# Kernel optimization log

Hardware: AMD Instinct MI355X
Metric: run time of the kernel (lower is better)

Reference implementation:

```python
import jax, jax.numpy as jnp
import numpy as np

H = 1024
B_SZ = 4
L = 2048


def setup_inputs() -> dict:
    key = jax.random.key(0)
    ks = jax.random.split(key, 7)
    s_in = 1.0 / np.sqrt(H)
    x = jax.random.normal(ks[0], (B_SZ, L, H), dtype=jnp.float32)
    # torch nn.Linear weights: (out_features, in_features)
    W_proj = jax.random.uniform(ks[1], (4 * H, H), minval=-s_in, maxval=s_in, dtype=jnp.float32)
    W_delta = jax.random.uniform(ks[2], (H, H), minval=-s_in, maxval=s_in, dtype=jnp.float32)
    b_delta = jax.random.uniform(ks[3], (H,), minval=-s_in, maxval=s_in, dtype=jnp.float32)
    A = 0.02 * jax.random.normal(ks[4], (1, 1, H), dtype=jnp.float32)
    Bp = 0.02 * jax.random.normal(ks[5], (1, H, 1), dtype=jnp.float32)
    D = jnp.ones((1,), dtype=jnp.float32)
    return {"x": x, "W_proj": W_proj, "A": A, "Bp": Bp, "D": D, "W_delta": W_delta, "b_delta": b_delta}


def reference(x, W_proj, A, Bp, D, W_delta, b_delta):
    # x: (b, l, h)
    h = x.shape[-1]
    proj = x @ W_proj.T                                   # (b, l, 4h)
    delta, Bs, Cs, residual = jnp.split(proj, 4, axis=-1) # each (b, l, h)
    delta = jax.nn.softplus(delta @ W_delta.T + b_delta)  # (b, l, h)
    A1 = A[0, 0]       # (h,)
    B1 = Bp[0, :, 0]   # (h,)
    # discretization: dA[b,h,l] = exp(delta*A)[b,l,h] * B1[h] (n-dim of Bp has size 1)
    dA = jnp.exp(delta * A1) * B1                         # (b, l, h), layout transposed vs torch
    # dB[b,h,0,l] = cumsum_l(delta[b,l,h] * B1[h])
    dB = jnp.cumsum(delta * B1, axis=1)                   # (b, l, h)
    # selective_scan: y[b,h,l] = sum_n (dA[b,h,l]*u[b,h,n] + dB[b,h,0,l]) * C[b,h,n]
    # sum over n distributes: y = dA * sum_n(u*C) + dB * sum_n(C)
    uC = jnp.sum(x * Cs, axis=1, keepdims=True)           # (b, 1, h)
    Csum = jnp.sum(Cs, axis=1, keepdims=True)             # (b, 1, h)
    y = dA * uC + dB * Csum                               # (b, l, h)
    return y + residual * D
```

## Files before the change

### kernel.cpp

```cpp
#include <hip/hip_runtime.h>
#include <hip/hip_bf16.h>
#include <cstdint>

#define H 1024
#define BSZ 4
#define LSEQ 2048
#define M_TOT (BSZ*LSEQ)
#define NCH 32
#define LCH (LSEQ/NCH)

typedef __attribute__((ext_vector_type(4))) float  f32x4;
typedef __attribute__((ext_vector_type(2))) float  f32x2;
typedef __attribute__((ext_vector_type(8))) __bf16 bf16x8;
typedef __attribute__((ext_vector_type(4))) __bf16 bf16x4;
typedef __attribute__((ext_vector_type(2))) __bf16 bf16x2;

typedef __attribute__((address_space(1))) unsigned int as1_u32;
typedef __attribute__((address_space(3))) unsigned int as3_u32;

__device__ __forceinline__ void gld_lds16(const void* g, const void* l) {
    as1_u32* gp = reinterpret_cast<as1_u32*>((uintptr_t)g);
    as3_u32* lp = reinterpret_cast<as3_u32*>((uint32_t)(uintptr_t)l);
    __builtin_amdgcn_global_load_lds(gp, lp, 16, 0, 0);
}

__device__ __forceinline__ float softplus_fast(float f) {
    return fmaxf(f, 0.f) + __logf(1.f + __expf(-fabsf(f)));
}

template<int KT, int MODE>
__global__ __launch_bounds__(256, 3) void gemm_bt(
    const __bf16* __restrict__ A,
    const __bf16* __restrict__ B,
    __bf16* __restrict__ O0)
{
    constexpr int K = KT * 32;
    __shared__ __align__(16) __bf16 lds[16384];

    const int tid  = threadIdx.x;
    const int lane = tid & 63;
    const int wid  = tid >> 6;
    const int wr   = (wid >> 1) * 64;
    const int wc   = (wid & 1) * 64;
    const int l15  = lane & 15;
    const int quad = lane >> 4;

    const int row0 = blockIdx.y * 128;
    const int col0 = blockIdx.x * 128;

    const int srow = lane >> 2;
    const int soct = (lane & 3) ^ ((lane >> 3) & 3);
    const __bf16* ag0 = A + (size_t)(row0 + (wid    )*16 + srow) * K + soct*8;
    const __bf16* ag1 = A + (size_t)(row0 + (wid + 4)*16 + srow) * K + soct*8;
    const __bf16* bg0 = B + (size_t)(col0 + (wid    )*16 + srow) * K + soct*8;
    const __bf16* bg1 = B + (size_t)(col0 + (wid + 4)*16 + srow) * K + soct*8;
    const int lA0 = (wid    )*512;
    const int lA1 = (wid + 4)*512;
    const int lB0 = 4096 + (wid    )*512;
    const int lB1 = 4096 + (wid + 4)*512;

    const int sw = (l15 >> 1) & 3;
    int aoff[4], boff[4];
#pragma unroll
    for (int i = 0; i < 4; ++i) {
        aoff[i] =        ((wr + i*16 + l15) * 4 + (quad ^ sw)) * 8;
        boff[i] = 4096 + ((wc + i*16 + l15) * 4 + (quad ^ sw)) * 8;
    }

    f32x4 acc[4][4] = {};

    auto stage = [&](int buf) {
        __bf16* base = lds + buf * 8192;
        gld_lds16(ag0, base + lA0);
        gld_lds16(ag1, base + lA1);
        gld_lds16(bg0, base + lB0);
        gld_lds16(bg1, base + lB1);
        ag0 += 32; ag1 += 32; bg0 += 32; bg1 += 32;
    };
    auto compute = [&](int buf) {
        const __bf16* base = lds + buf * 8192;
        bf16x8 af[4], bf[4];
#pragma unroll
        for (int i = 0; i < 4; ++i) af[i] = *(const bf16x8*)(base + aoff[i]);
#pragma unroll
        for (int j = 0; j < 4; ++j) bf[j] = *(const bf16x8*)(base + boff[j]);
#pragma unroll
        for (int i = 0; i < 4; ++i)
#pragma unroll
            for (int j = 0; j < 4; ++j)
                acc[i][j] = __builtin_amdgcn_mfma_f32_16x16x32_bf16(
                    af[i], bf[j], acc[i][j], 0, 0, 0);
    };

    stage(0);
#pragma unroll 2
    for (int kt = 0; kt < KT; ++kt) {
        __syncthreads();
        if (kt + 1 < KT) stage((kt + 1) & 1);
        compute(kt & 1);
    }

    const int colb = col0 + wc + l15;
    const int rowb = row0 + wr + quad*4;
#pragma unroll
    for (int i = 0; i < 4; ++i)
#pragma unroll
        for (int j = 0; j < 4; ++j) {
            const int col = colb + j*16;
#pragma unroll
            for (int r = 0; r < 4; ++r)
                O0[(size_t)(rowb + i*16 + r) * H + col] = (__bf16)acc[i][j][r];
        }
}


#define BAR()    asm volatile("s_barrier" ::: "memory")
#define WAIT6()  asm volatile("s_waitcnt vmcnt(6)" ::: "memory")
#define WAIT0()  asm volatile("s_waitcnt vmcnt(0)" ::: "memory")

#define STA(b,u,kt) gld_lds16(Asrc + (size_t)((u)*64)*H + (kt)*64, \
                              lds + (b)*24576 + (u)*4096 + lwb)
#define STB(b,u,kt) gld_lds16(Bsrc + (size_t)((u)*64)*H + (kt)*64, \
                              lds + (b)*24576 + 16384 + (u)*4096 + lwb)
#define STAGE6(b,kt) do { STA(b,0,kt); STA(b,1,kt); STA(b,2,kt); STA(b,3,kt); \
                          STB(b,0,kt); STB(b,1,kt); } while(0)

#define TILE(bc,bn,kn,DS,WAITMAC) do {                                        \
    WAITMAC();                                                                \
    BAR();                                                                    \
    { const __bf16* base_ = lds + (bc)*24576;                                 \
      _Pragma("unroll")                                                       \
      for (int i_ = 0; i_ < 4; ++i_)                                          \
          af0[i_] = *(const bf16x8*)(base_ + aoff[i_]);                       \
      _Pragma("unroll")                                                       \
      for (int j_ = 0; j_ < 4; ++j_)                                          \
          bf0[j_] = *(const bf16x8*)(base_ + boff[j_]); }                     \
    if (DS) STAGE6(bn, kn);                                                   \
    BAR();                                                                    \
    __builtin_amdgcn_s_setprio(1);                                            \
    _Pragma("unroll")                                                         \
    for (int i_ = 0; i_ < 4; ++i_)                                            \
    _Pragma("unroll")                                                         \
    for (int j_ = 0; j_ < 4; ++j_)                                            \
        acc[i_][j_] = __builtin_amdgcn_mfma_f32_16x16x32_bf16(                \
            af0[i_], bf0[j_], acc[i_][j_], 0, 0, 0);                          \
    __builtin_amdgcn_s_setprio(0);                                            \
    BAR();                                                                    \
    { const __bf16* base_ = lds + (bc)*24576;                                 \
      _Pragma("unroll")                                                       \
      for (int i_ = 0; i_ < 4; ++i_)                                          \
          af1[i_] = *(const bf16x8*)(base_ + (aoff[i_] ^ 32));                \
      _Pragma("unroll")                                                       \
      for (int j_ = 0; j_ < 4; ++j_)                                          \
          bf1[j_] = *(const bf16x8*)(base_ + (boff[j_] ^ 32)); }              \
    BAR();                                                                    \
    __builtin_amdgcn_s_setprio(1);                                            \
    _Pragma("unroll")                                                         \
    for (int i_ = 0; i_ < 4; ++i_)                                            \
    _Pragma("unroll")                                                         \
    for (int j_ = 0; j_ < 4; ++j_)                                            \
        acc[i_][j_] = __builtin_amdgcn_mfma_f32_16x16x32_bf16(                \
            af1[i_], bf1[j_], acc[i_][j_], 0, 0, 0);                          \
    __builtin_amdgcn_s_setprio(0);                                            \
} while(0)

__global__ __launch_bounds__(512, 2) void gemm256b(
    const __bf16* __restrict__ A,
    const __bf16* __restrict__ B,
    __bf16* __restrict__ O0,
    __bf16* __restrict__ O2,
    const __bf16* __restrict__ xb,
    const float* __restrict__ bias,
    float* __restrict__ pD,
    float* __restrict__ pUp,
    float* __restrict__ pCp)
{
    __shared__ __align__(16) __bf16 lds[73728];

    const int tid  = threadIdx.x;
    const int lane = tid & 63;
    const int wid  = tid >> 6;
    const int l15  = lane & 15;
    const int quad = lane >> 4;
    const int wrv  = (wid >> 1) * 64;
    const int wcv  = (wid & 1) * 64;

    const int bid = blockIdx.x;
    const int swz = (bid & 7) * 96 + (bid >> 3);
    const int bx = swz % 24;
    const int by = swz / 24;
    const int row0 = by * 256;
    const int col0 = bx * 128;

    const int lg = (tid & 7) ^ ((tid >> 3) & 7);
    const __bf16* Asrc = A + (size_t)(row0 + (tid >> 3)) * H + lg * 8;
    const __bf16* Bsrc = B + (size_t)(col0 + (tid >> 3)) * H + lg * 8;
    const int lwb = wid * 512;

    int aoff[4], boff[4];
#pragma unroll
    for (int i = 0; i < 4; ++i)
        aoff[i] = (wrv + i*16 + l15)*64 + ((quad ^ (l15 & 7)) << 3);
#pragma unroll
    for (int j = 0; j < 4; ++j)
        boff[j] = 16384 + (wcv + j*16 + l15)*64 + ((quad ^ (l15 & 7)) << 3);

    f32x4 acc[4][4] = {};
    bf16x8 af0[4], bf0[4], af1[4], bf1[4];

    STAGE6(0, 0);
    STAGE6(1, 1);

#pragma unroll 1
    for (int g = 0; g < 4; ++g) {
        TILE(0, 2, 3*g + 2, 1, WAIT6);
        TILE(1, 0, 3*g + 3, 1, WAIT6);
        TILE(2, 1, 3*g + 4, 1, WAIT6);
    }
    TILE(0, 2, 14, 1, WAIT6);
    TILE(1, 0, 15, 1, WAIT6);
    TILE(2, 0,  0, 0, WAIT6);
    TILE(0, 0,  0, 0, WAIT0);
    __syncthreads();

    const int seg   = col0 >> 10;
    const int cbase = col0 & 1023;
    const int colb  = cbase + wcv + l15;
    const int rowb  = row0 + wrv + quad*4;

    if (seg == 0) {
        const int chunk = (row0 + wrv) >> 6;
#pragma unroll
        for (int j = 0; j < 4; ++j) {
            const int col = colb + j*16;
            const float bv = bias[col];
            float s = 0.f;
#pragma unroll
            for (int i = 0; i < 4; ++i)
#pragma unroll
                for (int r = 0; r < 4; ++r) {
                    float f = softplus_fast(acc[i][j][r] + bv);
                    O0[(size_t)(rowb + i*16 + r) * H + col] = (__bf16)f;
                    s += f;
                }
            s += __shfl_down(s, 32); s += __shfl_down(s, 16);
            if (quad == 0) pD[chunk*H + col] = s;
        }
    } else if (seg == 2) {
#pragma unroll
        for (int i = 0; i < 4; ++i)
#pragma unroll
            for (int j = 0; j < 4; ++j) {
                const int col = colb + j*16;
#pragma unroll
                for (int r = 0; r < 4; ++r)
                    O2[(size_t)(rowb + i*16 + r) * H + col] = (__bf16)acc[i][j][r];
            }
    } else {
#pragma unroll
        for (int i = 0; i < 4; ++i)
#pragma unroll
            for (int j = 0; j < 4; ++j) {
                const int lcol = wcv + j*16 + l15;
#pragma unroll
                for (int r = 0; r < 4; ++r) {
                    const int lrow = wrv + i*16 + quad*4 + r;
                    lds[lrow*128 + (((lcol>>3) ^ (lrow&15)) << 3) + (lcol&7)]
                        = (__bf16)acc[i][j][r];
                }
            }
        __syncthreads();
        const int g = tid >> 4, oct = tid & 15;
        const int gc0 = cbase + oct*8;
        float su[8] = {}, sc[8] = {};
#pragma unroll
        for (int rr = 0; rr < 8; ++rr) {
            const int lrow = g*8 + rr;
            bf16x8 cv = *(const bf16x8*)(lds + lrow*128 +
                                         ((oct ^ (lrow&15)) << 3));
            bf16x8 xv = *(const bf16x8*)(xb + (size_t)(row0 + lrow)*H + gc0);
#pragma unroll
            for (int q = 0; q < 8; ++q) {
                float c = (float)cv[q];
                su[q] += (float)xv[q] * c;
                sc[q] += c;
            }
        }
        float* pf = reinterpret_cast<float*>(lds);
        __syncthreads();
#pragma unroll
        for (int q = 0; q < 8; ++q) {
            pf[g*128 + oct*8 + q]        = su[q];
            pf[4096 + g*128 + oct*8 + q] = sc[q];
        }
        __syncthreads();
        const int col = tid & 127;
        const int rb  = (tid >> 7) & 1;
        const int arr = tid >> 8;
        float s = 0.f;
#pragma unroll
        for (int g2 = 0; g2 < 16; ++g2)
            s += pf[arr*4096 + (rb*16 + g2)*128 + col];
        float* dst = arr ? pCp : pUp;
        dst[(size_t)((row0 >> 7) + rb)*H + cbase + col] = s;
    }
}

#define XB 8192
#define PB 2048
#define DB 1024
#define TB 256
__global__ void cast_kernel(const float* __restrict__ x,
                            const float* __restrict__ Wp,
                            const float* __restrict__ Wd,
                            __bf16* __restrict__ xb,
                            __bf16* __restrict__ Wpb,
                            __bf16* __restrict__ Wdb,
                            __bf16* __restrict__ Wp1T)
{
    __shared__ __bf16 tlds[64*65];
    const int t = threadIdx.x;
    const int bidx = blockIdx.x;

    if (bidx < XB + PB + DB) {
        const f32x4* src; __bf16* dst; int si, di;
        if (bidx < XB) {
            int i = bidx*256 + t;
            src = (const f32x4*)x;  si = i; dst = xb;  di = i;
        } else if (bidx < XB + PB) {
            int j = (bidx - XB)*256 + t;
            int row = j >> 8, cf = j & 255;
            src = (const f32x4*)Wp; si = (2048 + row)*256 + cf;
            dst = Wpb; di = (1024 + row)*256 + cf;
        } else {
            int j = (bidx - XB - PB)*256 + t;
            src = (const f32x4*)Wd; si = j; dst = Wdb; di = j;
        }
        f32x4 v = src[si];
        bf16x4 o = { (__bf16)v[0], (__bf16)v[1], (__bf16)v[2], (__bf16)v[3] };
        *(bf16x4*)(dst + (size_t)di*4) = o;
    } else {
        int tt = bidx - (XB + PB + DB);
        int ty = tt >> 4, tx = tt & 15;
        int rb = t >> 4, cb = t & 15;
#pragma unroll
        for (int rr = 0; rr < 4; ++rr) {
            int row = rb*4 + rr;
            f32x4 v = *(const f32x4*)(Wp + (size_t)(ty*64 + row)*1024 + tx*64 + cb*4);
#pragma unroll
            for (int q = 0; q < 4; ++q)
                tlds[row*65 + cb*4 + q] = (__bf16)v[q];
        }
        __syncthreads();
#pragma unroll
        for (int rr = 0; rr < 4; ++rr) {
            int kk = rb*4 + rr;
            bf16x4 o = { tlds[(cb*4+0)*65 + kk], tlds[(cb*4+1)*65 + kk],
                         tlds[(cb*4+2)*65 + kk], tlds[(cb*4+3)*65 + kk] };
            *(bf16x4*)(Wp1T + (size_t)(tx*64 + kk)*1024 + ty*64 + cb*4) = o;
        }
    }
}

__global__ void final_kernel(const __bf16* __restrict__ delta,
                             const __bf16* __restrict__ res,
                             const float* __restrict__ pD,
                             const float* __restrict__ pUp,
                             const float* __restrict__ pCp,
                             const float* __restrict__ Av,
                             const float* __restrict__ Bv,
                             const float* __restrict__ Dv,
                             float* __restrict__ out)
{
    const int c = blockIdx.x, b = blockIdx.z;
    const int h0 = blockIdx.y * 256 + threadIdx.x * 2;
    float run0 = 0.f, run1 = 0.f;
    for (int cp = 0; cp < c; ++cp) {
        f32x2 v = *(const f32x2*)(pD + (b*NCH + cp)*H + h0);
        run0 += v[0]; run1 += v[1];
    }
    float uc0 = 0.f, uc1 = 0.f, cs0 = 0.f, cs1 = 0.f;
#pragma unroll
    for (int i = 0; i < 16; ++i) {
        f32x2 u = *(const f32x2*)(pUp + (b*16 + i)*H + h0);
        f32x2 s = *(const f32x2*)(pCp + (b*16 + i)*H + h0);
        uc0 += u[0]; uc1 += u[1]; cs0 += s[0]; cs1 += s[1];
    }
    const f32x2 a1 = *(const f32x2*)(Av + h0);
    const f32x2 b1 = *(const f32x2*)(Bv + h0);
    const float dd = Dv[0];
    size_t base = ((size_t)(b*LSEQ + c*LCH)) * H + h0;
    for (int l = 0; l < LCH; ++l) {
        size_t idx = base + (size_t)l * H;
        bf16x2 dv2 = *(const bf16x2*)(delta + idx);
        bf16x2 rs2 = *(const bf16x2*)(res + idx);
        float d0 = (float)dv2[0], d1v = (float)dv2[1];
        run0 += d0; run1 += d1v;
        f32x2 o;
        o[0] = __expf(d0*a1[0])*b1[0]*uc0 + run0*b1[0]*cs0 + (float)rs2[0]*dd;
        o[1] = __expf(d1v*a1[1])*b1[1]*uc1 + run1*b1[1]*cs1 + (float)rs2[1]*dd;
        *(f32x2*)(out + idx) = o;
    }
}

extern "C" void kernel_launch(void* const* d_in, const int* in_sizes, int n_in,
                              void* d_out, int out_size, void* d_ws, size_t ws_size,
                              hipStream_t stream)
{
    (void)in_sizes; (void)n_in; (void)out_size; (void)ws_size;
    const float* x  = (const float*)d_in[0];
    const float* Wp = (const float*)d_in[1];
    const float* Av = (const float*)d_in[2];
    const float* Bv = (const float*)d_in[3];
    const float* Dv = (const float*)d_in[4];
    const float* Wd = (const float*)d_in[5];
    const float* bd = (const float*)d_in[6];
    float* out = (float*)d_out;

    char* ws = (char*)d_ws;
    size_t o = 0;
    auto alloc = [&](size_t bytes) {
        void* p = ws + o; o += (bytes + 255) & ~(size_t)255; return p;
    };
    __bf16* xb   = (__bf16*)alloc((size_t)M_TOT * H * 2);
    __bf16* Wpb  = (__bf16*)alloc((size_t)3072 * H * 2);
    __bf16* Wdb  = (__bf16*)alloc((size_t)H * H * 2);
    __bf16* Wp1T = (__bf16*)alloc((size_t)H * H * 2);
    __bf16* resb = (__bf16*)alloc((size_t)M_TOT * H * 2);
    __bf16* db   = (__bf16*)alloc((size_t)M_TOT * H * 2);
    float*  pD   = (float*)alloc((size_t)BSZ * NCH * H * 4);
    float*  pUp  = (float*)alloc((size_t)64 * H * 4);
    float*  pCp  = (float*)alloc((size_t)64 * H * 4);

    cast_kernel<<<XB + PB + DB + TB, 256, 0, stream>>>(
        x, Wp, Wd, xb, Wpb, Wdb, Wp1T);
    gemm_bt<32, 0><<<dim3(8, 8), 256, 0, stream>>>(Wdb, Wp1T, Wpb);
    gemm256b<<<dim3(768), 512, 0, stream>>>(
        xb, Wpb, db, resb, xb, bd, pD, pUp, pCp);
    final_kernel<<<dim3(NCH, 4, BSZ), 128, 0, stream>>>(db, resb, pD, pUp, pCp,
                                                        Av, Bv, Dv, out);
}
```

Before: 200.3 us.

## Shrink weight-fusion GEMM tiles and split scan epilogue into finer chunks

The small weight-fusion GEMM (W_delta times W_proj slice) goes from 64 blocks of 128x128 tiles to 256 blocks of 64x64 tiles, so more compute units are busy. The final scan kernel now uses 128 chunks of 16 rows instead of 32 chunks of 64, and the main GEMM epilogue writes delta partial sums per 16 rows. This raises parallelism in the memory-bound final pass and shortens its serial loop. The cost is a longer prefix loop over earlier partial sums, and the smaller GEMM tiles get less data reuse.

```diff
diff --git a/kernel.cpp b/kernel.cpp
--- a/kernel.cpp
+++ b/kernel.cpp
@@ -6,8 +6,8 @@
 #define BSZ 4
 #define LSEQ 2048
 #define M_TOT (BSZ*LSEQ)
-#define NCH 32
-#define LCH (LSEQ/NCH)
+#define NCH2 128
+#define LCH2 16
 
 typedef __attribute__((ext_vector_type(4))) float  f32x4;
 typedef __attribute__((ext_vector_type(2))) float  f32x2;
@@ -28,95 +28,59 @@
     return fmaxf(f, 0.f) + __logf(1.f + __expf(-fabsf(f)));
 }
 
-template<int KT, int MODE>
-__global__ __launch_bounds__(256, 3) void gemm_bt(
+#define BAR()    asm volatile("s_barrier" ::: "memory")
+#define WAIT6()  asm volatile("s_waitcnt vmcnt(6)" ::: "memory")
+#define WAIT0()  asm volatile("s_waitcnt vmcnt(0)" ::: "memory")
+
+__global__ __launch_bounds__(256) void wfuse_gemm(
     const __bf16* __restrict__ A,
     const __bf16* __restrict__ B,
-    __bf16* __restrict__ O0)
+    __bf16* __restrict__ O)
 {
-    constexpr int K = KT * 32;
-    __shared__ __align__(16) __bf16 lds[16384];
-
+    __shared__ __align__(16) __bf16 lds[2*4096];
     const int tid  = threadIdx.x;
     const int lane = tid & 63;
     const int wid  = tid >> 6;
-    const int wr   = (wid >> 1) * 64;
-    const int wc   = (wid & 1) * 64;
     const int l15  = lane & 15;
     const int quad = lane >> 4;
-
-    const int row0 = blockIdx.y * 128;
-    const int col0 = blockIdx.x * 128;
-
-    const int srow = lane >> 2;
-    const int soct = (lane & 3) ^ ((lane >> 3) & 3);
-    const __bf16* ag0 = A + (size_t)(row0 + (wid    )*16 + srow) * K + soct*8;
-    const __bf16* ag1 = A + (size_t)(row0 + (wid + 4)*16 + srow) * K + soct*8;
-    const __bf16* bg0 = B + (size_t)(col0 + (wid    )*16 + srow) * K + soct*8;
-    const __bf16* bg1 = B + (size_t)(col0 + (wid + 4)*16 + srow) * K + soct*8;
-    const int lA0 = (wid    )*512;
-    const int lA1 = (wid + 4)*512;
-    const int lB0 = 4096 + (wid    )*512;
-    const int lB1 = 4096 + (wid + 4)*512;
-
-    const int sw = (l15 >> 1) & 3;
-    int aoff[4], boff[4];
-#pragma unroll
-    for (int i = 0; i < 4; ++i) {
-        aoff[i] =        ((wr + i*16 + l15) * 4 + (quad ^ sw)) * 8;
-        boff[i] = 4096 + ((wc + i*16 + l15) * 4 + (quad ^ sw)) * 8;
-    }
-
-    f32x4 acc[4][4] = {};
-
-    auto stage = [&](int buf) {
-        __bf16* base = lds + buf * 8192;
-        gld_lds16(ag0, base + lA0);
-        gld_lds16(ag1, base + lA1);
-        gld_lds16(bg0, base + lB0);
-        gld_lds16(bg1, base + lB1);
-        ag0 += 32; ag1 += 32; bg0 += 32; bg1 += 32;
+    const int row0 = blockIdx.y * 64;
+    const int col0 = blockIdx.x * 64;
+
+    const __bf16* Asrc = A + (size_t)(row0 + (tid >> 2)) * 1024 + (tid & 3) * 8;
+    const __bf16* Bsrc = B + (size_t)(col0 + (tid >> 2)) * 1024 + (tid & 3) * 8;
+    const int ldst = (tid >> 2) * 32 + (tid & 3) * 8;
+
+    auto stage = [&](int buf, int kt) {
+        gld_lds16(Asrc + kt * 32, lds + buf * 4096 + ldst);
+        gld_lds16(Bsrc + kt * 32, lds + buf * 4096 + 2048 + ldst);
     };
-    auto compute = [&](int buf) {
-        const __bf16* base = lds + buf * 8192;
-        bf16x8 af[4], bf[4];
-#pragma unroll
-        for (int i = 0; i < 4; ++i) af[i] = *(const bf16x8*)(base + aoff[i]);
-#pragma unroll
-        for (int j = 0; j < 4; ++j) bf[j] = *(const bf16x8*)(base + boff[j]);
-#pragma unroll
-        for (int i = 0; i < 4; ++i)
-#pragma unroll
-            for (int j = 0; j < 4; ++j)
-                acc[i][j] = __builtin_amdgcn_mfma_f32_16x16x32_bf16(
-                    af[i], bf[j], acc[i][j], 0, 0, 0);
-    };
-
-    stage(0);
+
+    f32x4 acc[4] = {};
+    stage(0, 0);
 #pragma unroll 2
-    for (int kt = 0; kt < KT; ++kt) {
+    for (int kt = 0; kt < 32; ++kt) {
         __syncthreads();
-        if (kt + 1 < KT) stage((kt + 1) & 1);
-        compute(kt & 1);
-    }
-
-    const int colb = col0 + wc + l15;
-    const int rowb = row0 + wr + quad*4;
-#pragma unroll
-    for (int i = 0; i < 4; ++i)
-#pragma unroll
-        for (int j = 0; j < 4; ++j) {
-            const int col = colb + j*16;
-#pragma unroll
-            for (int r = 0; r < 4; ++r)
-                O0[(size_t)(rowb + i*16 + r) * H + col] = (__bf16)acc[i][j][r];
-        }
-}
-
-
-#define BAR()    asm volatile("s_barrier" ::: "memory")
-#define WAIT6()  asm volatile("s_waitcnt vmcnt(6)" ::: "memory")
-#define WAIT0()  asm volatile("s_waitcnt vmcnt(0)" ::: "memory")
+        if (kt + 1 < 32) stage((kt + 1) & 1, kt + 1);
+        const __bf16* base = lds + (kt & 1) * 4096;
+        bf16x8 a = *(const bf16x8*)(base + (wid * 16 + l15) * 32 + quad * 8);
+        bf16x8 b[4];
+#pragma unroll
+        for (int j = 0; j < 4; ++j)
+            b[j] = *(const bf16x8*)(base + 2048 + (j * 16 + l15) * 32 + quad * 8);
+#pragma unroll
+        for (int j = 0; j < 4; ++j)
+            acc[j] = __builtin_amdgcn_mfma_f32_16x16x32_bf16(a, b[j], acc[j], 0, 0, 0);
+    }
+
+    const int rowb = row0 + wid * 16 + quad * 4;
+#pragma unroll
+    for (int j = 0; j < 4; ++j) {
+        const int col = col0 + j * 16 + l15;
+#pragma unroll
+        for (int r = 0; r < 4; ++r)
+            O[(size_t)(rowb + r) * H + col] = (__bf16)acc[j][r];
+    }
+}
 
 #define STA(b,u,kt) gld_lds16(Asrc + (size_t)((u)*64)*H + (kt)*64, \
                               lds + (b)*24576 + (u)*4096 + lwb)
@@ -229,22 +193,23 @@
     const int rowb  = row0 + wrv + quad*4;
 
     if (seg == 0) {
-        const int chunk = (row0 + wrv) >> 6;
+        const int chunk16 = (row0 + wrv) >> 4;
 #pragma unroll
         for (int j = 0; j < 4; ++j) {
             const int col = colb + j*16;
             const float bv = bias[col];
-            float s = 0.f;
-#pragma unroll
-            for (int i = 0; i < 4; ++i)
+#pragma unroll
+            for (int i = 0; i < 4; ++i) {
+                float s = 0.f;
 #pragma unroll
                 for (int r = 0; r < 4; ++r) {
                     float f = softplus_fast(acc[i][j][r] + bv);
                     O0[(size_t)(rowb + i*16 + r) * H + col] = (__bf16)f;
                     s += f;
                 }
-            s += __shfl_down(s, 32); s += __shfl_down(s, 16);
-            if (quad == 0) pD[chunk*H + col] = s;
+                s += __shfl_down(s, 32); s += __shfl_down(s, 16);
+                if (quad == 0) pD[(size_t)(chunk16 + i)*H + col] = s;
+            }
         }
     } else if (seg == 2) {
 #pragma unroll
@@ -362,7 +327,8 @@
     }
 }
 
-__global__ void final_kernel(const __bf16* __restrict__ delta,
+__global__ __launch_bounds__(128) void final_kernel(
+                             const __bf16* __restrict__ delta,
                              const __bf16* __restrict__ res,
                              const float* __restrict__ pD,
                              const float* __restrict__ pUp,
@@ -375,8 +341,9 @@
     const int c = blockIdx.x, b = blockIdx.z;
     const int h0 = blockIdx.y * 256 + threadIdx.x * 2;
     float run0 = 0.f, run1 = 0.f;
+#pragma unroll 4
     for (int cp = 0; cp < c; ++cp) {
-        f32x2 v = *(const f32x2*)(pD + (b*NCH + cp)*H + h0);
+        f32x2 v = *(const f32x2*)(pD + (size_t)(b*NCH2 + cp)*H + h0);
         run0 += v[0]; run1 += v[1];
     }
     float uc0 = 0.f, uc1 = 0.f, cs0 = 0.f, cs1 = 0.f;
@@ -389,8 +356,9 @@
     const f32x2 a1 = *(const f32x2*)(Av + h0);
     const f32x2 b1 = *(const f32x2*)(Bv + h0);
     const float dd = Dv[0];
-    size_t base = ((size_t)(b*LSEQ + c*LCH)) * H + h0;
-    for (int l = 0; l < LCH; ++l) {
+    size_t base = ((size_t)(b*LSEQ + c*LCH2)) * H + h0;
+#pragma unroll 4
+    for (int l = 0; l < LCH2; ++l) {
         size_t idx = base + (size_t)l * H;
         bf16x2 dv2 = *(const bf16x2*)(delta + idx);
         bf16x2 rs2 = *(const bf16x2*)(res + idx);
@@ -428,15 +396,15 @@
     __bf16* Wp1T = (__bf16*)alloc((size_t)H * H * 2);
     __bf16* resb = (__bf16*)alloc((size_t)M_TOT * H * 2);
     __bf16* db   = (__bf16*)alloc((size_t)M_TOT * H * 2);
-    float*  pD   = (float*)alloc((size_t)BSZ * NCH * H * 4);
+    float*  pD   = (float*)alloc((size_t)BSZ * NCH2 * H * 4);
     float*  pUp  = (float*)alloc((size_t)64 * H * 4);
     float*  pCp  = (float*)alloc((size_t)64 * H * 4);
 
     cast_kernel<<<XB + PB + DB + TB, 256, 0, stream>>>(
         x, Wp, Wd, xb, Wpb, Wdb, Wp1T);
-    gemm_bt<32, 0><<<dim3(8, 8), 256, 0, stream>>>(Wdb, Wp1T, Wpb);
+    wfuse_gemm<<<dim3(16, 16), 256, 0, stream>>>(Wdb, Wp1T, Wpb);
     gemm256b<<<dim3(768), 512, 0, stream>>>(
         xb, Wpb, db, resb, xb, bd, pD, pUp, pCp);
-    final_kernel<<<dim3(NCH, 4, BSZ), 128, 0, stream>>>(db, resb, pD, pUp, pCp,
-                                                        Av, Bv, Dv, out);
-}
+    final_kernel<<<dim3(NCH2, 4, BSZ), 128, 0, stream>>>(db, resb, pD, pUp, pCp,
+                                                         Av, Bv, Dv, out);
+}
```

New measurement: 201.9 us. About the same (+0.8%).
